# Optimization experiments

Measured on AMD Instinct MI355X. Metric: run time of the kernel, lower is better.

Reference implementation:

```python
import jax, jax.numpy as jnp
from jax import lax
import numpy as np

B, T, D_IN, H = 64, 512, 256, 512  # batch, seq_len, input features, hidden size
G = 4 * H  # lstm gate dim


def setup_inputs() -> dict:
    key = jax.random.key(0)
    ks = jax.random.split(key, 14)
    s_in = 1.0 / np.sqrt(H)  # torch RNNCellBase init scale
    def w(k, shape):
        return jax.random.normal(k, shape, dtype=jnp.float32) * s_in
    def mask(k, shape):
        return (jax.random.uniform(k, shape) > 0.3).astype(jnp.float32)
    return {
        "x": jax.random.normal(ks[0], (B, T, D_IN), dtype=jnp.float32),
        "W_ih0": w(ks[1], (G, D_IN)), "W_hh0": w(ks[2], (G, H)),
        "b_ih0": w(ks[3], (G,)), "b_hh0": w(ks[4], (G,)),
        "m_ih0": mask(ks[5], (G, D_IN)), "m_hh0": mask(ks[6], (G, H)),
        "W_ih1": w(ks[7], (G, H)), "W_hh1": w(ks[8], (G, H)),
        "b_ih1": w(ks[9], (G,)), "b_hh1": w(ks[10], (G,)),
        "m_ih1": mask(ks[11], (G, H)), "m_hh1": mask(ks[12], (G, H)),
    }


def _lstm_layer(x, W_ih, W_hh, b_ih, b_hh):
    # x: [B, T, D]; masked weights precomputed once (mask is constant over time)
    b = x.shape[0]
    h_dim = W_hh.shape[1]
    # precompute input projection for all timesteps: [T, B, 4H]
    xW = jnp.einsum('btd,gd->tbg', x, W_ih) + b_ih + b_hh

    def step(carry, xt):
        h, c = carry
        gates = xt + h @ W_hh.T  # [B, 4H]
        i, f, g, o = jnp.split(gates, 4, axis=-1)
        c = jax.nn.sigmoid(f) * c + jax.nn.sigmoid(i) * jnp.tanh(g)
        h = jax.nn.sigmoid(o) * jnp.tanh(c)
        return (h, c), h

    h0 = jnp.zeros((b, h_dim), x.dtype)
    (_, _), hs = lax.scan(step, (h0, h0), xW)  # hs: [T, B, H]
    return jnp.swapaxes(hs, 0, 1)  # [B, T, H]


def reference(x, W_ih0, W_hh0, b_ih0, b_hh0, m_ih0, m_hh0,
              W_ih1, W_hh1, b_ih1, b_hh1, m_ih1, m_hh1):
    out = _lstm_layer(x, W_ih0 * m_ih0, W_hh0 * m_hh0, b_ih0, b_hh0)
    out = _lstm_layer(out, W_ih1 * m_ih1, W_hh1 * m_hh1, b_ih1, b_hh1)
    return out[:, -1, :]  # batch_first=True -> last timestep hidden [B, H]
```

## Files before the change

kernel.cpp:

```cpp
#include <hip/hip_runtime.h>
#include <cstdint>


typedef _Float16 f16;
typedef _Float16 half8 __attribute__((ext_vector_type(8)));
typedef float floatx4 __attribute__((ext_vector_type(4)));

#define B_ 64
#define T_ 512
#define DIN_ 256
#define H_ 512
#define G_ 2048

static const size_t OFF_FLAGS = 0;
static const size_t OFF_H0B   = 32768;
static const size_t OFF_H1B   = OFF_H0B + 524288;
static const size_t OFF_WIH0  = OFF_H1B + 131072;
static const size_t OFF_WHH0  = OFF_WIH0 + (size_t)G_ * DIN_ * 2;
static const size_t OFF_WIH1  = OFF_WHH0 + (size_t)G_ * H_ * 2;
static const size_t OFF_WHH1  = OFF_WIH1 + (size_t)G_ * H_ * 2;
static const size_t OFF_B0    = OFF_WHH1 + (size_t)G_ * H_ * 2;
static const size_t OFF_B1    = OFF_B0 + 8192;
static const size_t OFF_XF16  = OFF_B1 + 8192;
static const size_t XF16_BYTES = (size_t)8 * T_ * 8 * DIN_ * 2;
static const size_t ZERO_BYTES = OFF_WIH0;

__device__ __forceinline__ uint32_t ald(const uint32_t* p) {
    return __hip_atomic_load(p, __ATOMIC_RELAXED, __HIP_MEMORY_SCOPE_AGENT);
}
__device__ __forceinline__ void ast(uint32_t* p, uint32_t v) {
    __hip_atomic_store(p, v, __ATOMIC_RELAXED, __HIP_MEMORY_SCOPE_AGENT);
}

__device__ __forceinline__ half8 mload(const float* w, const float* m) {
    const float4 a = *(const float4*)w, b = *(const float4*)(w + 4);
    const float4 c = *(const float4*)m, d = *(const float4*)(m + 4);
    half8 h = { (f16)(a.x * c.x), (f16)(a.y * c.y), (f16)(a.z * c.z), (f16)(a.w * c.w),
                (f16)(b.x * d.x), (f16)(b.y * d.y), (f16)(b.z * d.z), (f16)(b.w * d.w) };
    return h;
}

__global__ void k_prep(const float* __restrict__ x, f16* __restrict__ xf16,
                       const float* __restrict__ Wih0, const float* __restrict__ Mih0,
                       const float* __restrict__ Whh0, const float* __restrict__ Mhh0,
                       const float* __restrict__ bih0, const float* __restrict__ bhh0,
                       const float* __restrict__ Wih1, const float* __restrict__ Mih1,
                       const float* __restrict__ Whh1, const float* __restrict__ Mhh1,
                       const float* __restrict__ bih1, const float* __restrict__ bhh1,
                       f16* __restrict__ wih0, f16* __restrict__ whh0,
                       f16* __restrict__ wih1, f16* __restrict__ whh1,
                       float* __restrict__ bs0, float* __restrict__ bs1) {
    const int bid = blockIdx.x, tid = threadIdx.x;
    if (bid < 4096) {
        if (!xf16) return;
        const int isl = bid & 7, t = bid >> 3;
        const int b = tid >> 5, dq = tid & 31;
        const float* s = x + ((size_t)(isl * 8 + b) * T_ + t) * DIN_ + dq * 8;
        const float4 a  = *(const float4*)s;
        const float4 bb = *(const float4*)(s + 4);
        half8 h = { (f16)a.x, (f16)a.y, (f16)a.z, (f16)a.w,
                    (f16)bb.x, (f16)bb.y, (f16)bb.z, (f16)bb.w };
        *(half8*)(xf16 + ((size_t)(isl * 512 + t) * 8 + b) * 256 + dq * 8) = h;
    } else if (bid < 4352) {
        const int i = (bid - 4096) * 256 + tid;
        ((half8*)wih0)[i] = mload(Wih0 + (size_t)i * 8, Mih0 + (size_t)i * 8);
    } else if (bid < 4864) {
        const int i = (bid - 4352) * 256 + tid;
        ((half8*)whh0)[i] = mload(Whh0 + (size_t)i * 8, Mhh0 + (size_t)i * 8);
    } else if (bid < 5376) {
        const int i = (bid - 4864) * 256 + tid;
        ((half8*)wih1)[i] = mload(Wih1 + (size_t)i * 8, Mih1 + (size_t)i * 8);
    } else if (bid < 5888) {
        const int i = (bid - 5376) * 256 + tid;
        ((half8*)whh1)[i] = mload(Whh1 + (size_t)i * 8, Mhh1 + (size_t)i * 8);
    } else {
        const int i = (bid - 5888) * 256 + tid;
        if (i < G_) bs0[i] = bih0[i] + bhh0[i];
        else        bs1[i - G_] = bih1[i - G_] + bhh1[i - G_];
    }
}

__device__ __forceinline__ void poll_flags(const uint32_t* ownF, uint32_t town,
                                           const uint32_t* crossF, uint32_t tcr,
                                           int lane) {
    const uint32_t* p = (lane < 32) ? (ownF + (size_t)lane * 16)
                                    : (crossF + (size_t)(lane - 32) * 16);
    const uint32_t tgt = (lane < 32) ? town : tcr;
    while (true) {
        const uint32_t v = ald(p);
        if (__all((int)(v >= tgt))) break;
        __builtin_amdgcn_s_sleep(1);
    }
}

__device__ __forceinline__ float lstm_cell(float gi, float gf, float gg, float go,
                                           float& c) {
    const float i_ = 1.f / (1.f + __expf(-gi));
    const float f_ = 1.f / (1.f + __expf(-gf));
    const float gc = fminf(fmaxf(gg, -20.f), 20.f);
    const float e2 = __expf(2.f * gc);
    const float g_ = (e2 - 1.f) / (e2 + 1.f);
    const float o_ = 1.f / (1.f + __expf(-go));
    c = f_ * c + i_ * g_;
    const float cc  = fminf(fmaxf(c, -20.f), 20.f);
    const float e2c = __expf(2.f * cc);
    return o_ * (e2c - 1.f) / (e2c + 1.f);
}

__global__ __launch_bounds__(256, 2) void fused_rnn(
    const float* __restrict__ x,
    const f16* __restrict__ xf16,
    const f16* __restrict__ Wih0, const f16* __restrict__ Whh0,
    const float* __restrict__ bs0,
    const f16* __restrict__ Wih1, const f16* __restrict__ Whh1,
    const float* __restrict__ bs1,
    float* __restrict__ dout,
    uint32_t* __restrict__ h0b,
    uint32_t* __restrict__ h1b,
    uint32_t* __restrict__ flags)
{
    __shared__ f16 bl0[8][520];
    __shared__ f16 bl1[8][520];
    __shared__ float glp[4][4][16][9];

    const int tid  = threadIdx.x;
    const int bid  = blockIdx.x;
    const int isl  = bid & 7;
    const int mem  = (bid >> 3) & 31;
    const int layer = bid >> 8;
    const int jb = mem * 16, b0 = isl * 8;
    const int wave = tid >> 6, lane = tid & 63, lm = lane & 15, quad = lane >> 4;
    const int eb = tid >> 4, ejj = tid & 15;
    const int hrow = lm < 8 ? lm : 7;

    uint32_t* ownF   = flags + (size_t)(layer * 8 + isl) * 512;
    uint32_t* crossF = flags + (size_t)((1 - layer) * 8 + isl) * 512;
    uint32_t* h0i = h0b + (size_t)isl * 8 * 2048;
    uint32_t* h1i = h1b + (size_t)isl * 2 * 2048;

    if (layer == 0) {
        half8 ah[4][4], ai[4][2];
        {
            const int kb  = wave * 128 + quad * 8;
            const int kbx = wave * 64 + quad * 8;
#pragma unroll
            for (int gt = 0; gt < 4; ++gt) {
                const f16* wr = Whh0 + (size_t)(gt * 512 + jb + lm) * H_ + kb;
                const f16* xr = Wih0 + (size_t)(gt * 512 + jb + lm) * DIN_ + kbx;
#pragma unroll
                for (int kk = 0; kk < 4; ++kk) ah[gt][kk] = *(const half8*)(wr + kk * 32);
#pragma unroll
                for (int kk = 0; kk < 2; ++kk) ai[gt][kk] = *(const half8*)(xr + kk * 32);
            }
        }
        float bias[4];
#pragma unroll
        for (int g = 0; g < 4; ++g) bias[g] = bs0[g * 512 + jb + ejj];
        float c = 0.f;
        const f16* xs = xf16 ? (xf16 + (size_t)isl * T_ * 2048 +
                                (tid >> 5) * 256 + (tid & 31) * 8)
                             : nullptr;
        const float* xp = x + (size_t)(b0 + (tid >> 5)) * T_ * DIN_ + (tid & 31) * 8;
        half8 xcur;
        if (xs) {
            xcur = *(const half8*)xs;
        } else {
            const float4 a = *(const float4*)xp;
            const float4 b = *(const float4*)(xp + 4);
            xcur = { (f16)a.x, (f16)a.y, (f16)a.z, (f16)a.w,
                     (f16)b.x, (f16)b.y, (f16)b.z, (f16)b.w };
        }

        for (int t = 0; t < T_; ++t) {
            *(half8*)&bl1[tid >> 5][(tid & 31) * 8] = xcur;
            {
                const int tn = t + 1 < T_ ? t + 1 : t;
                if (xs) {
                    xcur = *(const half8*)(xs + (size_t)tn * 2048);
                } else {
                    const float4 a = *(const float4*)(xp + (size_t)tn * DIN_);
                    const float4 b = *(const float4*)(xp + (size_t)tn * DIN_ + 4);
                    xcur = { (f16)a.x, (f16)a.y, (f16)a.z, (f16)a.w,
                             (f16)b.x, (f16)b.y, (f16)b.z, (f16)b.w };
                }
            }
            if (wave == 0)
                poll_flags(ownF, (uint32_t)t, crossF,
                           t >= 7 ? (uint32_t)(t - 7) : 0u, lane);
            __syncthreads();
            uint32_t va[8];
            {
                const uint32_t* hb = h0i + (size_t)((t + 7) & 7) * 2048;
#pragma unroll
                for (int i = 0; i < 8; ++i) va[i] = ald(hb + i * 256 + tid);
            }
            floatx4 acc[4] = {};
            {
                const f16* br1 = &bl1[hrow][wave * 64 + quad * 8];
#pragma unroll
                for (int kk = 0; kk < 2; ++kk) {
                    const half8 bv = *(const half8*)(br1 + kk * 32);
#pragma unroll
                    for (int gt = 0; gt < 4; ++gt)
                        acc[gt] = __builtin_amdgcn_mfma_f32_16x16x32_f16(
                            ai[gt][kk], bv, acc[gt], 0, 0, 0);
                }
            }
            __builtin_amdgcn_sched_barrier(0);
#pragma unroll
            for (int i = 0; i < 8; ++i) {
                const int u = i * 256 + tid;
                *(uint32_t*)&bl0[u >> 8][(u & 255) * 2] = va[i];
            }
            __syncthreads();
            {
                const f16* br0 = &bl0[hrow][wave * 128 + quad * 8];
#pragma unroll
                for (int kk = 0; kk < 4; ++kk) {
                    const half8 bv = *(const half8*)(br0 + kk * 32);
#pragma unroll
                    for (int gt = 0; gt < 4; ++gt)
                        acc[gt] = __builtin_amdgcn_mfma_f32_16x16x32_f16(
                            ah[gt][kk], bv, acc[gt], 0, 0, 0);
                }
            }
            if (lm < 8)
#pragma unroll
                for (int gt = 0; gt < 4; ++gt)
#pragma unroll
                    for (int r = 0; r < 4; ++r)
                        glp[wave][gt][quad * 4 + r][lm] = acc[gt][r];
            __syncthreads();
            if (tid < 128) {
                float gi = bias[0], gf = bias[1], gg = bias[2], go = bias[3];
#pragma unroll
                for (int w = 0; w < 4; ++w) {
                    gi += glp[w][0][ejj][eb]; gf += glp[w][1][ejj][eb];
                    gg += glp[w][2][ejj][eb]; go += glp[w][3][ejj][eb];
                }
                const float hn = lstm_cell(gi, gf, gg, go, c);
                const float ho = __shfl_xor(hn, 1);
                if (!(ejj & 1)) {
                    union { f16 h[2]; uint32_t u; } pk;
                    pk.h[0] = (f16)hn; pk.h[1] = (f16)ho;
                    ast(h0i + (size_t)(t & 7) * 2048 + (eb * H_ + jb + ejj) / 2, pk.u);
                }
            }
            __syncthreads();
            if (tid == 0) ast(ownF + mem * 16, (uint32_t)(t + 1));
        }
    } else {
        half8 ah[4][4], ai[4][4];
        {
            const int kb = wave * 128 + quad * 8;
#pragma unroll
            for (int gt = 0; gt < 4; ++gt) {
                const f16* wr = Whh1 + (size_t)(gt * 512 + jb + lm) * H_ + kb;
                const f16* xr = Wih1 + (size_t)(gt * 512 + jb + lm) * H_ + kb;
#pragma unroll
                for (int kk = 0; kk < 4; ++kk) {
                    ah[gt][kk] = *(const half8*)(wr + kk * 32);
                    ai[gt][kk] = *(const half8*)(xr + kk * 32);
                }
            }
        }
        float bias[4];
#pragma unroll
        for (int g = 0; g < 4; ++g) bias[g] = bs1[g * 512 + jb + ejj];
        float c = 0.f;

        uint32_t vb[8];
        if (wave == 0) poll_flags(ownF, 0u, crossF, 1u, lane);
        __syncthreads();
#pragma unroll
        for (int i = 0; i < 8; ++i) vb[i] = ald(h0i + i * 256 + tid);

        for (int t = 0; t < T_; ++t) {
#pragma unroll
            for (int i = 0; i < 8; ++i) {
                const int u = i * 256 + tid;
                *(uint32_t*)&bl1[u >> 8][(u & 255) * 2] = vb[i];
            }
            if (wave == 0)
                poll_flags(ownF, (uint32_t)t, crossF,
                           (uint32_t)(t + 2 < T_ ? t + 2 : T_), lane);
            __syncthreads();
            uint32_t va[8];
            {
                const uint32_t* hb = h1i + (size_t)((t + 1) & 1) * 2048;
#pragma unroll
                for (int i = 0; i < 8; ++i) va[i] = ald(hb + i * 256 + tid);
                const uint32_t* gb = h0i + (size_t)((t + 1) & 7) * 2048;
#pragma unroll
                for (int i = 0; i < 8; ++i) vb[i] = ald(gb + i * 256 + tid);
            }
            floatx4 acc[4] = {};
            {
                const f16* br1 = &bl1[hrow][wave * 128 + quad * 8];
#pragma unroll
                for (int kk = 0; kk < 4; ++kk) {
                    const half8 bv = *(const half8*)(br1 + kk * 32);
#pragma unroll
                    for (int gt = 0; gt < 4; ++gt)
                        acc[gt] = __builtin_amdgcn_mfma_f32_16x16x32_f16(
                            ai[gt][kk], bv, acc[gt], 0, 0, 0);
                }
            }
            __builtin_amdgcn_sched_barrier(0);
#pragma unroll
            for (int i = 0; i < 8; ++i) {
                const int u = i * 256 + tid;
                *(uint32_t*)&bl0[u >> 8][(u & 255) * 2] = va[i];
            }
            __syncthreads();
            {
                const f16* br0 = &bl0[hrow][wave * 128 + quad * 8];
#pragma unroll
                for (int kk = 0; kk < 4; ++kk) {
                    const half8 bv = *(const half8*)(br0 + kk * 32);
#pragma unroll
                    for (int gt = 0; gt < 4; ++gt)
                        acc[gt] = __builtin_amdgcn_mfma_f32_16x16x32_f16(
                            ah[gt][kk], bv, acc[gt], 0, 0, 0);
                }
            }
            if (lm < 8)
#pragma unroll
                for (int gt = 0; gt < 4; ++gt)
#pragma unroll
                    for (int r = 0; r < 4; ++r)
                        glp[wave][gt][quad * 4 + r][lm] = acc[gt][r];
            __syncthreads();
            if (tid < 128) {
                float gi = bias[0], gf = bias[1], gg = bias[2], go = bias[3];
#pragma unroll
                for (int w = 0; w < 4; ++w) {
                    gi += glp[w][0][ejj][eb]; gf += glp[w][1][ejj][eb];
                    gg += glp[w][2][ejj][eb]; go += glp[w][3][ejj][eb];
                }
                const float hn = lstm_cell(gi, gf, gg, go, c);
                const float ho = __shfl_xor(hn, 1);
                if (!(ejj & 1)) {
                    union { f16 h[2]; uint32_t u; } pk;
                    pk.h[0] = (f16)hn; pk.h[1] = (f16)ho;
                    ast(h1i + (size_t)(t & 1) * 2048 + (eb * H_ + jb + ejj) / 2, pk.u);
                }
                if (t == T_ - 1)
                    dout[(size_t)(b0 + eb) * H_ + jb + ejj] = hn;
            }
            __syncthreads();
            if (tid == 0) ast(ownF + mem * 16, (uint32_t)(t + 1));
        }
    }
}

extern "C" void kernel_launch(void* const* d_in, const int* in_sizes, int n_in,
                              void* d_out, int out_size, void* d_ws, size_t ws_size,
                              hipStream_t stream) {
    const float* x    = (const float*)d_in[0];
    const float* Wih0 = (const float*)d_in[1];
    const float* Whh0 = (const float*)d_in[2];
    const float* bih0 = (const float*)d_in[3];
    const float* bhh0 = (const float*)d_in[4];
    const float* mih0 = (const float*)d_in[5];
    const float* mhh0 = (const float*)d_in[6];
    const float* Wih1 = (const float*)d_in[7];
    const float* Whh1 = (const float*)d_in[8];
    const float* bih1 = (const float*)d_in[9];
    const float* bhh1 = (const float*)d_in[10];
    const float* mih1 = (const float*)d_in[11];
    const float* mhh1 = (const float*)d_in[12];

    char* ws = (char*)d_ws;
    uint32_t* flags = (uint32_t*)(ws + OFF_FLAGS);
    uint32_t* h0b   = (uint32_t*)(ws + OFF_H0B);
    uint32_t* h1b   = (uint32_t*)(ws + OFF_H1B);
    f16*   wih0 = (f16*)(ws + OFF_WIH0);
    f16*   whh0 = (f16*)(ws + OFF_WHH0);
    f16*   wih1 = (f16*)(ws + OFF_WIH1);
    f16*   whh1 = (f16*)(ws + OFF_WHH1);
    float* bs0  = (float*)(ws + OFF_B0);
    float* bs1  = (float*)(ws + OFF_B1);
    const bool has_xf = (ws_size >= OFF_XF16 + XF16_BYTES);
    f16*   xf16 = has_xf ? (f16*)(ws + OFF_XF16) : (f16*)nullptr;
    float* out  = (float*)d_out;

    hipMemsetAsync(ws, 0, ZERO_BYTES, stream);

    k_prep<<<5904, 256, 0, stream>>>(x, xf16,
                                     Wih0, mih0, Whh0, mhh0, bih0, bhh0,
                                     Wih1, mih1, Whh1, mhh1, bih1, bhh1,
                                     wih0, whh0, wih1, whh1, bs0, bs1);

    fused_rnn<<<512, 256, 0, stream>>>(x, xf16, wih0, whh0, bs0,
                                       wih1, whh1, bs1,
                                       out, h0b, h1b, flags);

    (void)in_sizes; (void)n_in; (void)out_size;
}
```

Baseline: 1.014 ms.

## Distribute flag polling across threads and move next-step loads into idle waves

The single wave-0 poll-then-barrier at the top of each step is replaced. Each thread now polls only the own-layer peer flag it depends on, and the cross-layer poll runs in waves that are idle during the LSTM cell phase. The next timestep's x tile (layer 0) and layer-0 hidden state (layer 1) are loaded into shared memory by idle waves after the GEMM, which removes one barrier per step and overlaps the loads with the elementwise work. The cross-layer lag target changes from t+2 to t+3, and correctness now depends on the shared buffer being rewritten only after every wave has read it.

```diff
diff --git a/kernel.cpp b/kernel.cpp
--- a/kernel.cpp
+++ b/kernel.cpp
@@ -80,19 +80,6 @@
     }
 }
 
-__device__ __forceinline__ void poll_flags(const uint32_t* ownF, uint32_t town,
-                                           const uint32_t* crossF, uint32_t tcr,
-                                           int lane) {
-    const uint32_t* p = (lane < 32) ? (ownF + (size_t)lane * 16)
-                                    : (crossF + (size_t)(lane - 32) * 16);
-    const uint32_t tgt = (lane < 32) ? town : tcr;
-    while (true) {
-        const uint32_t v = ald(p);
-        if (__all((int)(v >= tgt))) break;
-        __builtin_amdgcn_s_sleep(1);
-    }
-}
-
 __device__ __forceinline__ float lstm_cell(float gi, float gf, float gg, float go,
                                            float& c) {
     const float i_ = 1.f / (1.f + __expf(-gi));
@@ -105,6 +92,15 @@
     const float cc  = fminf(fmaxf(c, -20.f), 20.f);
     const float e2c = __expf(2.f * cc);
     return o_ * (e2c - 1.f) / (e2c + 1.f);
+}
+
+__device__ __forceinline__ void xpoll(const uint32_t* crossF, uint32_t tgt, int lane) {
+    const uint32_t* p = crossF + (size_t)(lane & 31) * 16;
+    while (true) {
+        const uint32_t v = ald(p);
+        if (__all((int)(v >= tgt))) break;
+        __builtin_amdgcn_s_sleep(1);
+    }
 }
 
 __global__ __launch_bounds__(256, 2) void fused_rnn(
@@ -138,6 +134,9 @@
     uint32_t* h0i = h0b + (size_t)isl * 8 * 2048;
     uint32_t* h1i = h1b + (size_t)isl * 2 * 2048;
 
+    const uint32_t* myf = ownF + (size_t)(tid >> 3) * 16;
+    const bool notown = (tid >> 3) != mem;
+
     if (layer == 0) {
         half8 ah[4][4], ai[4][2];
         {
@@ -157,37 +156,28 @@
 #pragma unroll
         for (int g = 0; g < 4; ++g) bias[g] = bs0[g * 512 + jb + ejj];
         float c = 0.f;
-        const f16* xs = xf16 ? (xf16 + (size_t)isl * T_ * 2048 +
-                                (tid >> 5) * 256 + (tid & 31) * 8)
-                             : nullptr;
-        const float* xp = x + (size_t)(b0 + (tid >> 5)) * T_ * DIN_ + (tid & 31) * 8;
-        half8 xcur;
-        if (xs) {
-            xcur = *(const half8*)xs;
+        const f16* xfi = xf16 ? (xf16 + (size_t)isl * T_ * 2048) : (const f16*)nullptr;
+
+        if (xfi) {
+            *(half8*)&bl1[tid >> 5][(tid & 31) * 8] =
+                *(const half8*)(xfi + (tid >> 5) * 256 + (tid & 31) * 8);
         } else {
+            const float* xp = x + (size_t)(b0 + (tid >> 5)) * T_ * DIN_ + (tid & 31) * 8;
             const float4 a = *(const float4*)xp;
             const float4 b = *(const float4*)(xp + 4);
-            xcur = { (f16)a.x, (f16)a.y, (f16)a.z, (f16)a.w,
-                     (f16)b.x, (f16)b.y, (f16)b.z, (f16)b.w };
-        }
+            half8 h = { (f16)a.x, (f16)a.y, (f16)a.z, (f16)a.w,
+                        (f16)b.x, (f16)b.y, (f16)b.z, (f16)b.w };
+            *(half8*)&bl1[tid >> 5][(tid & 31) * 8] = h;
+        }
+        __syncthreads();
 
         for (int t = 0; t < T_; ++t) {
-            *(half8*)&bl1[tid >> 5][(tid & 31) * 8] = xcur;
-            {
-                const int tn = t + 1 < T_ ? t + 1 : t;
-                if (xs) {
-                    xcur = *(const half8*)(xs + (size_t)tn * 2048);
-                } else {
-                    const float4 a = *(const float4*)(xp + (size_t)tn * DIN_);
-                    const float4 b = *(const float4*)(xp + (size_t)tn * DIN_ + 4);
-                    xcur = { (f16)a.x, (f16)a.y, (f16)a.z, (f16)a.w,
-                             (f16)b.x, (f16)b.y, (f16)b.z, (f16)b.w };
-                }
-            }
-            if (wave == 0)
-                poll_flags(ownF, (uint32_t)t, crossF,
-                           t >= 7 ? (uint32_t)(t - 7) : 0u, lane);
-            __syncthreads();
+            if (notown) {
+                const uint32_t f0 = ald(myf);
+                if (f0 < (uint32_t)t)
+                    while (ald(myf) < (uint32_t)t) __builtin_amdgcn_s_sleep(1);
+            }
+            __builtin_amdgcn_sched_barrier(0);
             uint32_t va[8];
             {
                 const uint32_t* hb = h0i + (size_t)((t + 7) & 7) * 2048;
@@ -245,6 +235,30 @@
                     pk.h[0] = (f16)hn; pk.h[1] = (f16)ho;
                     ast(h0i + (size_t)(t & 7) * 2048 + (eb * H_ + jb + ejj) / 2, pk.u);
                 }
+            } else if (wave == 2) {
+                const int tn = t + 1 < T_ ? t + 1 : t;
+                if (xfi) {
+                    const f16* src = xfi + (size_t)tn * 2048;
+#pragma unroll
+                    for (int j = 0; j < 4; ++j) {
+                        const int o = j * 512 + lane * 8;
+                        *(half8*)&bl1[o >> 8][o & 255] = *(const half8*)(src + o);
+                    }
+                } else {
+#pragma unroll
+                    for (int j = 0; j < 4; ++j) {
+                        const int o = j * 512 + lane * 8;
+                        const float* s = x + (size_t)(b0 + (o >> 8)) * T_ * DIN_
+                                           + (size_t)tn * DIN_ + (o & 255);
+                        const float4 a = *(const float4*)s;
+                        const float4 b2 = *(const float4*)(s + 4);
+                        half8 h = { (f16)a.x, (f16)a.y, (f16)a.z, (f16)a.w,
+                                    (f16)b2.x, (f16)b2.y, (f16)b2.z, (f16)b2.w };
+                        *(half8*)&bl1[o >> 8][o & 255] = h;
+                    }
+                }
+            } else {
+                xpoll(crossF, t >= 7 ? (uint32_t)(t - 7) : 0u, lane);
             }
             __syncthreads();
             if (tid == 0) ast(ownF + mem * 16, (uint32_t)(t + 1));
@@ -269,30 +283,33 @@
         for (int g = 0; g < 4; ++g) bias[g] = bs1[g * 512 + jb + ejj];
         float c = 0.f;
 
-        uint32_t vb[8];
-        if (wave == 0) poll_flags(ownF, 0u, crossF, 1u, lane);
-        __syncthreads();
-#pragma unroll
-        for (int i = 0; i < 8; ++i) vb[i] = ald(h0i + i * 256 + tid);
-
-        for (int t = 0; t < T_; ++t) {
+        {
+            const uint32_t* cf = crossF + (size_t)(tid >> 3) * 16;
+            while (ald(cf) < 2u) __builtin_amdgcn_s_sleep(1);
+            __builtin_amdgcn_sched_barrier(0);
+            uint32_t vb[8];
+#pragma unroll
+            for (int i = 0; i < 8; ++i) vb[i] = ald(h0i + i * 256 + tid);
 #pragma unroll
             for (int i = 0; i < 8; ++i) {
                 const int u = i * 256 + tid;
                 *(uint32_t*)&bl1[u >> 8][(u & 255) * 2] = vb[i];
             }
-            if (wave == 0)
-                poll_flags(ownF, (uint32_t)t, crossF,
-                           (uint32_t)(t + 2 < T_ ? t + 2 : T_), lane);
-            __syncthreads();
+        }
+        __syncthreads();
+
+        for (int t = 0; t < T_; ++t) {
+            if (notown) {
+                const uint32_t f0 = ald(myf);
+                if (f0 < (uint32_t)t)
+                    while (ald(myf) < (uint32_t)t) __builtin_amdgcn_s_sleep(1);
+            }
+            __builtin_amdgcn_sched_barrier(0);
             uint32_t va[8];
             {
                 const uint32_t* hb = h1i + (size_t)((t + 1) & 1) * 2048;
 #pragma unroll
                 for (int i = 0; i < 8; ++i) va[i] = ald(hb + i * 256 + tid);
-                const uint32_t* gb = h0i + (size_t)((t + 1) & 7) * 2048;
-#pragma unroll
-                for (int i = 0; i < 8; ++i) vb[i] = ald(gb + i * 256 + tid);
             }
             floatx4 acc[4] = {};
             {
@@ -347,6 +364,26 @@
                 }
                 if (t == T_ - 1)
                     dout[(size_t)(b0 + eb) * H_ + jb + ejj] = hn;
+            } else {
+                if (t + 1 < T_) {
+                    const uint32_t* gb = h0i + (size_t)((t + 1) & 7) * 2048;
+                    const int jb4 = (wave == 2) ? 0 : 4;
+#pragma unroll
+                    for (int j = 0; j < 4; ++j) {
+                        const int d0 = (jb4 + j) * 256 + lane;
+                        const uint32_t w0 = ald(gb + d0);
+                        const uint32_t w1 = ald(gb + d0 + 64);
+                        const uint32_t w2 = ald(gb + d0 + 128);
+                        const uint32_t w3 = ald(gb + d0 + 192);
+                        *(uint32_t*)&bl1[jb4 + j][lane * 2]         = w0;
+                        *(uint32_t*)&bl1[jb4 + j][(lane + 64) * 2]  = w1;
+                        *(uint32_t*)&bl1[jb4 + j][(lane + 128) * 2] = w2;
+                        *(uint32_t*)&bl1[jb4 + j][(lane + 192) * 2] = w3;
+                    }
+                }
+                if (wave == 3) {
+                    xpoll(crossF, (uint32_t)(t + 3 < T_ ? t + 3 : T_), lane);
+                }
             }
             __syncthreads();
             if (tid == 0) ast(ownF + mem * 16, (uint32_t)(t + 1));
```

After: 1.898 ms. 1.87x slower.
